# Optimization experiments

Measured on AMD Instinct MI355X. Metric: run time of the kernel, lower is better.

The kernel has to match this reference:

```python
import jax, jax.numpy as jnp
import numpy as np

N_GROUPS = 32  # getGroupSize(.) assumed -> channels // 8 (or //24 for 3*ch) == 32 for ch=256
HEADS = 4


def group_norm(x, gamma, beta, groups=N_GROUPS, eps=1e-5):
    n, c = x.shape
    xg = x.reshape(n, groups, c // groups)
    mu = xg.mean(-1, keepdims=True)
    var = xg.var(-1, keepdims=True)
    xn = ((xg - mu) * jax.lax.rsqrt(var + eps)).reshape(n, c)
    return xn * gamma + beta


def setup_inputs():
    key = jax.random.key(0)
    N, E, CH, HID = 2000, 16000, 256, 256
    ks = jax.random.split(key, 24)

    def w(k, shape, s=0.02):
        return (jax.random.normal(k, shape) * s).astype(jnp.float32)

    inp = {
        'x': jax.random.normal(ks[0], (N, CH), jnp.float32),
        'edge_index': jax.random.randint(ks[1], (2, E), 0, N),
        'edge_attr': jax.random.normal(ks[2], (E, CH), jnp.float32),
        # edge_mlp: GN(3ch)+ReLU -> Linear(3ch,hid) -> GN(hid)+ReLU -> Linear(hid,ch)
        'gn_e1_g': jnp.ones((3 * CH,), jnp.float32), 'gn_e1_b': jnp.zeros((3 * CH,), jnp.float32),
        'We1': w(ks[3], (3 * CH, HID)), 'be1': jnp.zeros((HID,), jnp.float32),
        'gn_e2_g': jnp.ones((HID,), jnp.float32), 'gn_e2_b': jnp.zeros((HID,), jnp.float32),
        'We2': w(ks[4], (HID, CH)), 'be2': jnp.zeros((CH,), jnp.float32),
        # actN: GN(ch)+ReLU
        'gn_n_g': jnp.ones((CH,), jnp.float32), 'gn_n_b': jnp.zeros((CH,), jnp.float32),
        # multi-head attention projections
        'Wq': w(ks[5], (CH, CH)), 'bq': jnp.zeros((CH,), jnp.float32),
        'Wk': w(ks[6], (CH, CH)), 'bk': jnp.zeros((CH,), jnp.float32),
        'Wv': w(ks[7], (CH, CH)), 'bv': jnp.zeros((CH,), jnp.float32),
        'Wo': w(ks[8], (CH, CH)), 'bo': jnp.zeros((CH,), jnp.float32),
        # node_mlp: Linear(2ch,hid) -> GN(hid)+ReLU -> Linear(hid,ch)
        'Wn1': w(ks[9], (2 * CH, HID)), 'bn1': jnp.zeros((HID,), jnp.float32),
        'gn_n2_g': jnp.ones((HID,), jnp.float32), 'gn_n2_b': jnp.zeros((HID,), jnp.float32),
        'Wn2': w(ks[10], (HID, CH)), 'bn2': jnp.zeros((CH,), jnp.float32),
    }
    return inp


def reference(x, edge_index, edge_attr,
              gn_e1_g, gn_e1_b, We1, be1, gn_e2_g, gn_e2_b, We2, be2,
              gn_n_g, gn_n_b, Wq, bq, Wk, bk, Wv, bv, Wo, bo,
              Wn1, bn1, gn_n2_g, gn_n2_b, Wn2, bn2):
    row, col = edge_index[0], edge_index[1]
    N, ch = x.shape
    E = edge_attr.shape[0]
    dk = ch // HEADS

    # ---- edge model: cat(src, tgt, e) -> GN/ReLU -> Lin -> GN/ReLU -> Lin (+res) ----
    e_in = jnp.concatenate([x[row], x[col], edge_attr], axis=1)  # [E, 3ch]
    h = jax.nn.relu(group_norm(e_in, gn_e1_g, gn_e1_b))
    h = h @ We1 + be1
    h = jax.nn.relu(group_norm(h, gn_e2_g, gn_e2_b))
    e_out = h @ We2 + be2 + edge_attr  # [E, ch]

    # ---- node model: dense-masked MHA, queries=nodes, keys/values=edges ----
    mask = jnp.zeros((N, E), x.dtype).at[col, jnp.arange(E)].set(1.0)  # scatter adjacency
    q = (x @ Wq + bq).reshape(N, HEADS, dk)
    k = (e_out @ Wk + bk).reshape(E, HEADS, dk)
    v = (e_out @ Wv + bv).reshape(E, HEADS, dk)
    scores = jnp.einsum('nhd,ehd->hne', q, k) / jnp.sqrt(jnp.float32(dk))  # [H, N, E]
    scores = jnp.where(mask[None] > 0, scores, jnp.float32(-1e9))
    attn = jax.nn.softmax(scores, axis=-1)
    g = jnp.einsum('hne,ehd->nhd', attn, v).reshape(N, ch) @ Wo + bo  # [N, ch]

    xa = jax.nn.relu(group_norm(x, gn_n_g, gn_n_b))
    h = jnp.concatenate([xa, g], axis=1) @ Wn1 + bn1  # thinker='cat'
    h = jax.nn.relu(group_norm(h, gn_n2_g, gn_n2_b))
    n_out = h @ Wn2 + bn2 + x  # residual

    return n_out, e_out
```

## Files before the change

### kernel.cpp

```cpp
#include <hip/hip_runtime.h>
#include <hip/hip_bf16.h>
#include <stdint.h>
#include <math.h>

#define CH 256

typedef __attribute__((ext_vector_type(8)))  short short8;
typedef __attribute__((ext_vector_type(16))) short short16;
typedef __attribute__((ext_vector_type(4)))  float f32x4;

#define GL2LDS16(g, l) __builtin_amdgcn_global_load_lds(                       \
    (const __attribute__((address_space(1))) void*)(g),                        \
    (__attribute__((address_space(3))) void*)(l), 16, 0, 0)

__device__ inline short f2bf(float f) {
    __hip_bfloat16 h = __float2bfloat16(f);
    short s;
    __builtin_memcpy(&s, &h, 2);
    return s;
}

__device__ inline float bf2f(short s) {
    unsigned u = ((unsigned)(unsigned short)s) << 16;
    float f;
    __builtin_memcpy(&f, &u, 4);
    return f;
}

__device__ inline float warp_sum64(float v) {
    v += __shfl_xor(v, 32, 64);
    v += __shfl_xor(v, 16, 64);
    v += __shfl_xor(v, 8, 64);
    v += __shfl_xor(v, 4, 64);
    v += __shfl_xor(v, 2, 64);
    v += __shfl_xor(v, 1, 64);
    return v;
}

__device__ inline float warp_max64(float v) {
    v = fmaxf(v, __shfl_xor(v, 32, 64));
    v = fmaxf(v, __shfl_xor(v, 16, 64));
    v = fmaxf(v, __shfl_xor(v, 8, 64));
    v = fmaxf(v, __shfl_xor(v, 4, 64));
    v = fmaxf(v, __shfl_xor(v, 2, 64));
    v = fmaxf(v, __shfl_xor(v, 1, 64));
    return v;
}

struct GArgs {
    const short* A; const short* Bt; const float* bias; const float* res;
    float* C; short* Cbf;
    const float* gamma; const float* beta; float* vbar;
    int M, K, Nc, ldc, coff;
    const short* A2; const short* Bt2; const float* bias2; short* Cbf2;
    int M2, Nc2, y_split;
    const float* x; const float* eattr; const int* rowi; const int* coli;
    const float* mu; const float* rs; const float* vg; const float* vbt;
};

template <int BM, int BN, int AMODE, int EPI, int DUAL, int VB>
__global__ __launch_bounds__(256) void mfma_gemm(GArgs g)
{
    constexpr int BK = 64;
    constexpr int AK = AMODE ? (BK + 8) : BK;
    constexpr int HM = BM / 2, HN = BN / 2;
    constexpr int FM = HM / 16, FN = HN / 16;
    constexpr int PA = BM / 32;
    constexpr int PB = BN / 32;
    __shared__ short As[BM * AK];
    __shared__ short Bs[BN * BK];
    __shared__ int sidx[AMODE ? 2 * BM : 1];

    const short* A = g.A; const short* Bt = g.Bt;
    const float* bias = g.bias; const float* res = g.res;
    float* C = g.C; short* Cbf = g.Cbf;
    int M = g.M, ldc = g.ldc, co = g.coff;
    const int K = g.K;
    int by = blockIdx.y, bx = blockIdx.x;
    bool qrole = false;
    if constexpr (DUAL) {
        if (by >= g.y_split) {
            by -= g.y_split;
            if (bx * BN >= g.Nc2) return;
            qrole = true;
            A = g.A2; Bt = g.Bt2; bias = g.bias2; Cbf = g.Cbf2;
            C = nullptr; res = nullptr;
            M = g.M2; ldc = g.Nc2; co = 0;
        }
    }

    const int t = threadIdx.x;
    const int wave = t >> 6, lane = t & 63;
    const int q = lane >> 4, l16 = lane & 15;
    const int row0 = by * BM;
    const int col0 = bx * BN;
    const int wm = wave & 1, wn = wave >> 1;

    if constexpr (AMODE) {
        if (t < BM) {
            int gr = row0 + t; if (gr >= M) gr = M - 1;
            sidx[t] = g.rowi[gr];
            sidx[BM + t] = g.coli[gr];
        }
        __syncthreads();
    }

    f32x4 acc[FM][FN];
    #pragma unroll
    for (int i = 0; i < FM; i++)
        #pragma unroll
        for (int j = 0; j < FN; j++) acc[i][j] = (f32x4){0.f, 0.f, 0.f, 0.f};

    for (int k0 = 0; k0 < K; k0 += BK) {
        if constexpr (AMODE == 1) {
            int reg = k0 >> 8;
            int rloc = t >> 3;
            int cpos = (t & 7) * 8;
            int pos = k0 + cpos;
            int G = pos / 24;
            float4 ga  = *(const float4*)&g.vg[pos];
            float4 ga2 = *(const float4*)&g.vg[pos + 4];
            float4 gb  = *(const float4*)&g.vbt[pos];
            float4 gb2 = *(const float4*)&g.vbt[pos + 4];
            int off = pos & 255;
            #pragma unroll
            for (int p = 0; p < BM / 32; p++) {
                int r2 = p * 32 + rloc;
                int e = row0 + r2; if (e >= M) e = M - 1;
                const float* srow;
                if (reg == 0)      srow = g.x + (size_t)sidx[r2] * CH;
                else if (reg == 1) srow = g.x + (size_t)sidx[BM + r2] * CH;
                else               srow = g.eattr + (size_t)e * CH;
                float4 va  = *(const float4*)&srow[off];
                float4 vb4 = *(const float4*)&srow[off + 4];
                float mm = g.mu[(size_t)e * 32 + G];
                float rr = g.rs[(size_t)e * 32 + G];
                short8 o;
                o[0] = f2bf(fmaxf((va.x - mm) * rr * ga.x + gb.x, 0.f));
                o[1] = f2bf(fmaxf((va.y - mm) * rr * ga.y + gb.y, 0.f));
                o[2] = f2bf(fmaxf((va.z - mm) * rr * ga.z + gb.z, 0.f));
                o[3] = f2bf(fmaxf((va.w - mm) * rr * ga.w + gb.w, 0.f));
                o[4] = f2bf(fmaxf((vb4.x - mm) * rr * ga2.x + gb2.x, 0.f));
                o[5] = f2bf(fmaxf((vb4.y - mm) * rr * ga2.y + gb2.y, 0.f));
                o[6] = f2bf(fmaxf((vb4.z - mm) * rr * ga2.z + gb2.z, 0.f));
                o[7] = f2bf(fmaxf((vb4.w - mm) * rr * ga2.w + gb2.w, 0.f));
                *(short8*)&As[r2 * AK + cpos] = o;
            }
        } else {
            #pragma unroll
            for (int p = 0; p < PA; p++) {
                int chunk = p * 256 + t;
                int r = chunk >> 3;
                int cs = (((chunk & 7) ^ (r & 7)) * 8);
                int gr = row0 + r; if (gr >= M) gr = M - 1;
                const short* gsrc = A + (size_t)gr * K + k0 + cs;
                short* ldst = &As[(p * 256 + wave * 64) * 8];
                GL2LDS16(gsrc, ldst);
            }
        }
        #pragma unroll
        for (int p = 0; p < PB; p++) {
            int chunk = p * 256 + t;
            int r = chunk >> 3;
            int cs = (((chunk & 7) ^ (r & 7)) * 8);
            const short* gsrc = Bt + (size_t)(col0 + r) * K + k0 + cs;
            short* ldst = &Bs[(p * 256 + wave * 64) * 8];
            GL2LDS16(gsrc, ldst);
        }
        __syncthreads();
        #pragma unroll
        for (int ks = 0; ks < 2; ks++) {
            short8 af[FM], bf[FN];
            #pragma unroll
            for (int mi = 0; mi < FM; mi++) {
                int R = wm * HM + mi * 16 + l16;
                if constexpr (AMODE == 1)
                    af[mi] = *(const short8*)&As[R * AK + ks * 32 + q * 8];
                else {
                    int slot = ((ks * 4 + q) ^ (R & 7)) * 8;
                    af[mi] = *(const short8*)&As[R * BK + slot];
                }
            }
            #pragma unroll
            for (int ni = 0; ni < FN; ni++) {
                int R = wn * HN + ni * 16 + l16;
                int slot = ((ks * 4 + q) ^ (R & 7)) * 8;
                bf[ni] = *(const short8*)&Bs[R * BK + slot];
            }
            #pragma unroll
            for (int mi = 0; mi < FM; mi++)
                #pragma unroll
                for (int ni = 0; ni < FN; ni++)
                    acc[mi][ni] = __builtin_amdgcn_mfma_f32_16x16x32_bf16(
                        af[mi], bf[ni], acc[mi][ni], 0, 0, 0);
        }
        __syncthreads();
    }

    #pragma unroll
    for (int ni = 0; ni < FN; ni++) {
        int cg = col0 + wn * HN + ni * 16 + l16;
        float bv = bias[cg];
        if constexpr (EPI == 1) {
            float ga = g.gamma[cg], be = g.beta[cg];
            #pragma unroll
            for (int mi = 0; mi < FM; mi++) {
                #pragma unroll
                for (int r = 0; r < 4; r++) {
                    float v = acc[mi][ni][r] + bv;
                    float s = v, sq = v * v;
                    s += __shfl_xor(s, 1, 64);  sq += __shfl_xor(sq, 1, 64);
                    s += __shfl_xor(s, 2, 64);  sq += __shfl_xor(sq, 2, 64);
                    s += __shfl_xor(s, 4, 64);  sq += __shfl_xor(sq, 4, 64);
                    float mean = s * 0.125f;
                    float var = sq * 0.125f - mean * mean;
                    float o = fmaxf((v - mean) * rsqrtf(var + 1e-5f) * ga + be, 0.f);
                    int rg = row0 + wm * HM + mi * 16 + q * 4 + r;
                    if (rg < M) Cbf[(size_t)rg * ldc + co + cg] = f2bf(o);
                }
            }
        } else {
            #pragma unroll
            for (int mi = 0; mi < FM; mi++) {
                #pragma unroll
                for (int r = 0; r < 4; r++) {
                    int rg = row0 + wm * HM + mi * 16 + q * 4 + r;
                    if (rg < M) {
                        float v = acc[mi][ni][r] + bv;
                        if (res) v += res[(size_t)rg * ldc + co + cg];
                        if (C)   C[(size_t)rg * ldc + co + cg] = v;
                        if (Cbf) Cbf[(size_t)rg * ldc + co + cg] = f2bf(v);
                    }
                }
            }
            if constexpr (VB) {
                if (!qrole && cg >= 256) {
                    float part = 0.f;
                    #pragma unroll
                    for (int mi = 0; mi < FM; mi++)
                        #pragma unroll
                        for (int r = 0; r < 4; r++) {
                            int rg = row0 + wm * HM + mi * 16 + q * 4 + r;
                            if (rg < M) part += acc[mi][ni][r] + bv;
                        }
                    part += __shfl_xor(part, 16, 64);
                    part += __shfl_xor(part, 32, 64);
                    if (q == 0) atomicAdd(&g.vbar[cg - 256], part);
                }
            }
        }
    }
}

struct PrepPack {
    const float* wsrc[8];
    short* wdst[8];
    int wK[8];
    int wstart[8];
    int NW, NP;
    const float* x;
    short* x_bf;
    short* cat_bf;
    float2* xs;
    const float* gng;
    const float* gnb;
    float* vbar;
    const float* bk;
    const float* bv;
    float* bkv;
    int* counts;
    int N;
};

__global__ __launch_bounds__(256) void prep_kernel(PrepPack p)
{
    int bid = blockIdx.x;
    int t = threadIdx.x;
    if (bid < p.NW) {
        int m = 0;
        #pragma unroll
        for (int i = 1; i < 8; i++) if (bid >= p.wstart[i]) m = i;
        int k0 = (bid - p.wstart[m]) * 16;
        const float* src = p.wsrc[m];
        short16 o;
        #pragma unroll
        for (int j = 0; j < 16; j++) o[j] = f2bf(src[(size_t)(k0 + j) * 256 + t]);
        *(short16*)(p.wdst[m] + (size_t)t * p.wK[m] + k0) = o;
        return;
    }
    if (bid >= p.NW + p.NP) {
        int i = (bid - p.NW - p.NP) * 256 + t;
        if (i < p.N) p.counts[i] = 0;
        return;
    }
    int pb = bid - p.NW;
    if (pb == 0) {
        p.vbar[t] = 0.f;
        p.bkv[t] = p.bk[t];
        p.bkv[256 + t] = p.bv[t];
    }
    int r = pb * 8 + (t >> 5);
    int g = t & 31;
    if (r >= p.N) return;
    size_t xb = (size_t)r * CH + g * 8;
    float4 a = *(const float4*)&p.x[xb];
    float4 b = *(const float4*)&p.x[xb + 4];
    short8 xr;
    xr[0] = f2bf(a.x); xr[1] = f2bf(a.y); xr[2] = f2bf(a.z); xr[3] = f2bf(a.w);
    xr[4] = f2bf(b.x); xr[5] = f2bf(b.y); xr[6] = f2bf(b.z); xr[7] = f2bf(b.w);
    *(short8*)&p.x_bf[xb] = xr;
    float s  = a.x + a.y + a.z + a.w + b.x + b.y + b.z + b.w;
    float s2 = a.x*a.x + a.y*a.y + a.z*a.z + a.w*a.w
             + b.x*b.x + b.y*b.y + b.z*b.z + b.w*b.w;
    p.xs[(size_t)r * 32 + g] = make_float2(s, s2);
    float m = s * 0.125f;
    float var = s2 * 0.125f - m * m;
    float rsd = rsqrtf(var + 1e-5f);
    float4 g0 = *(const float4*)&p.gng[g * 8];
    float4 g1 = *(const float4*)&p.gng[g * 8 + 4];
    float4 b0 = *(const float4*)&p.gnb[g * 8];
    float4 b1 = *(const float4*)&p.gnb[g * 8 + 4];
    short8 o;
    o[0] = f2bf(fmaxf((a.x - m) * rsd * g0.x + b0.x, 0.f));
    o[1] = f2bf(fmaxf((a.y - m) * rsd * g0.y + b0.y, 0.f));
    o[2] = f2bf(fmaxf((a.z - m) * rsd * g0.z + b0.z, 0.f));
    o[3] = f2bf(fmaxf((a.w - m) * rsd * g0.w + b0.w, 0.f));
    o[4] = f2bf(fmaxf((b.x - m) * rsd * g1.x + b1.x, 0.f));
    o[5] = f2bf(fmaxf((b.y - m) * rsd * g1.y + b1.y, 0.f));
    o[6] = f2bf(fmaxf((b.z - m) * rsd * g1.z + b1.z, 0.f));
    o[7] = f2bf(fmaxf((b.w - m) * rsd * g1.w + b1.w, 0.f));
    *(short8*)&p.cat_bf[(size_t)r * (2 * CH) + g * 8] = o;
}

__global__ __launch_bounds__(256) void estats_kernel(
    const float* __restrict__ eattr, const int* __restrict__ rowi,
    const int* __restrict__ coli, const float2* __restrict__ xs,
    float* __restrict__ mu, float* __restrict__ rs,
    int* __restrict__ counts, int E)
{
    __shared__ float2 ea[8][32];
    int t = threadIdx.x;
    int slot = t >> 5, g = t & 31;
    int e = blockIdx.x * 8 + slot;
    float4 a = *(const float4*)&eattr[(size_t)e * CH + g * 8];
    float4 b = *(const float4*)&eattr[(size_t)e * CH + g * 8 + 4];
    float s  = a.x + a.y + a.z + a.w + b.x + b.y + b.z + b.w;
    float s2 = a.x*a.x + a.y*a.y + a.z*a.z + a.w*a.w
             + b.x*b.x + b.y*b.y + b.z*b.z + b.w*b.w;
    ea[slot][g] = make_float2(s, s2);
    int r = rowi[e], c = coli[e];
    if (g == 0) atomicAdd(&counts[c], 1);
    __syncthreads();
    float S = 0.f, S2 = 0.f;
    #pragma unroll
    for (int j = 0; j < 3; j++) {
        int b3 = 3 * g + j;
        int src = b3 >> 5, idx = b3 & 31;
        float2 v;
        if (src == 0)      v = xs[(size_t)r * 32 + idx];
        else if (src == 1) v = xs[(size_t)c * 32 + idx];
        else               v = ea[slot][idx];
        S += v.x; S2 += v.y;
    }
    float m = S * (1.f / 24.f);
    float var = S2 * (1.f / 24.f) - m * m;
    mu[(size_t)e * 32 + g] = m;
    rs[(size_t)e * 32 + g] = rsqrtf(var + 1e-5f);
}

__global__ __launch_bounds__(1024) void scan_kernel(
    const int* __restrict__ counts, int* __restrict__ offsets,
    int* __restrict__ cursor, int N)
{
    __shared__ int s[1024];
    int t = threadIdx.x;
    int a = (2 * t     < N) ? counts[2 * t]     : 0;
    int b = (2 * t + 1 < N) ? counts[2 * t + 1] : 0;
    s[t] = a + b;
    __syncthreads();
    for (int off = 1; off < 1024; off <<= 1) {
        int v = (t >= off) ? s[t - off] : 0;
        __syncthreads();
        s[t] += v;
        __syncthreads();
    }
    int excl = (t > 0) ? s[t - 1] : 0;
    if (2 * t < N)     { offsets[2 * t]     = excl;     cursor[2 * t]     = excl; }
    if (2 * t + 1 < N) { offsets[2 * t + 1] = excl + a; cursor[2 * t + 1] = excl + a; }
    if (t == 1023) offsets[N] = s[1023];
}

__global__ __launch_bounds__(256) void escore_kernel(
    const short* __restrict__ qb, const short* __restrict__ kvb,
    const int* __restrict__ coli, int* __restrict__ cursor,
    int* __restrict__ elist, float* __restrict__ sc, int E)
{
    int e = blockIdx.x * 4 + (threadIdx.x >> 6);
    int lane = threadIdx.x & 63;
    if (e >= E) return;
    int c = coli[e];
    if (lane == 0) { int p = atomicAdd(&cursor[c], 1); elist[p] = e; }
    const short* qrow = qb + (size_t)c * CH;
    const short* krow = kvb + (size_t)e * 512;
    float d0 = bf2f(qrow[lane])       * bf2f(krow[lane]);
    float d1 = bf2f(qrow[64 + lane])  * bf2f(krow[64 + lane]);
    float d2 = bf2f(qrow[128 + lane]) * bf2f(krow[128 + lane]);
    float d3 = bf2f(qrow[192 + lane]) * bf2f(krow[192 + lane]);
    d0 = warp_sum64(d0);
    d1 = warp_sum64(d1);
    d2 = warp_sum64(d2);
    d3 = warp_sum64(d3);
    if (lane == 0) {
        float4 o = {d0 * 0.125f, d1 * 0.125f, d2 * 0.125f, d3 * 0.125f};
        *(float4*)&sc[(size_t)e * 4] = o;
    }
}

__global__ __launch_bounds__(256) void attn_kernel(
    const float* __restrict__ sc, const short* __restrict__ kvb,
    const int* __restrict__ offsets, const int* __restrict__ elist,
    const float* __restrict__ vbar, short* __restrict__ g_bf, int N, int E)
{
    int n = blockIdx.x;
    int h = threadIdx.x >> 6;
    int lane = threadIdx.x & 63;
    int s0 = offsets[n], s1 = offsets[n + 1];
    float out = 0.f;
    if (s1 > s0) {
        float m = -INFINITY, l = 0.f;
        for (int base = s0; base < s1; base += 64) {
            int cn = s1 - base; if (cn > 64) cn = 64;
            int e = (lane < cn) ? elist[base + lane] : 0;
            float s = (lane < cn) ? sc[(size_t)e * 4 + h] : -INFINITY;
            float mc = warp_max64(s);
            float nm = fmaxf(m, mc);
            float scale = __expf(m - nm);
            float pp = (lane < cn) ? __expf(s - nm) : 0.f;
            float ps = warp_sum64(pp);
            l = l * scale + ps;
            out *= scale;
            m = nm;
            for (int i = 0; i < cn; i++) {
                float pi = __shfl(pp, i, 64);
                int   ei = __shfl(e, i, 64);
                out += pi * bf2f(kvb[(size_t)ei * 512 + 256 + h * 64 + lane]);
            }
        }
        out /= l;
    } else {
        out = vbar[h * 64 + lane] * (1.f / (float)E);
    }
    g_bf[(size_t)n * CH + h * 64 + lane] = f2bf(out);
}

extern "C" void kernel_launch(void* const* d_in, const int* in_sizes, int n_in,
                              void* d_out, int out_size, void* d_ws, size_t ws_size,
                              hipStream_t stream)
{
    const float* x       = (const float*)d_in[0];
    const int*   ei      = (const int*)d_in[1];
    const float* eattr   = (const float*)d_in[2];
    const float* gn_e1_g = (const float*)d_in[3];
    const float* gn_e1_b = (const float*)d_in[4];
    const float* We1     = (const float*)d_in[5];
    const float* be1     = (const float*)d_in[6];
    const float* gn_e2_g = (const float*)d_in[7];
    const float* gn_e2_b = (const float*)d_in[8];
    const float* We2     = (const float*)d_in[9];
    const float* be2     = (const float*)d_in[10];
    const float* gn_n_g  = (const float*)d_in[11];
    const float* gn_n_b  = (const float*)d_in[12];
    const float* Wq      = (const float*)d_in[13];
    const float* bq      = (const float*)d_in[14];
    const float* Wk      = (const float*)d_in[15];
    const float* bk      = (const float*)d_in[16];
    const float* Wv      = (const float*)d_in[17];
    const float* bv      = (const float*)d_in[18];
    const float* Wo      = (const float*)d_in[19];
    const float* bo      = (const float*)d_in[20];
    const float* Wn1     = (const float*)d_in[21];
    const float* bn1     = (const float*)d_in[22];
    const float* gn_n2_g = (const float*)d_in[23];
    const float* gn_n2_b = (const float*)d_in[24];
    const float* Wn2     = (const float*)d_in[25];
    const float* bn2     = (const float*)d_in[26];

    const int N = in_sizes[0] / CH;
    const int E = in_sizes[2] / CH;

    float* nout = (float*)d_out;
    float* eout = (float*)d_out + (size_t)N * CH;

    char* base = (char*)d_ws;
    short* kv_bf  = (short*)base; base += (size_t)E * 512 * 2;
    short* h2_bf  = (short*)base; base += (size_t)E * CH * 2;
    short* eo_bf  = (short*)base; base += (size_t)E * CH * 2;
    short* q_bf   = (short*)base; base += (size_t)N * CH * 2;
    short* g_bf   = (short*)base; base += (size_t)N * CH * 2;
    short* cat_bf = (short*)base; base += (size_t)N * 2 * CH * 2;
    short* hn_bf  = (short*)base; base += (size_t)N * CH * 2;
    short* x_bf   = (short*)base; base += (size_t)N * CH * 2;
    float2* xs    = (float2*)base; base += (size_t)N * 32 * 8;
    float* mub    = (float*)base; base += (size_t)E * 32 * 4;
    float* rsb    = (float*)base; base += (size_t)E * 32 * 4;
    float* sc     = (float*)base; base += (size_t)E * 4 * 4;
    float* vbar   = (float*)base; base += 1024;
    float* bkv    = (float*)base; base += 2048;
    short* We1t = (short*)base; base += (size_t)768 * 256 * 2;
    short* We2t = (short*)base; base += (size_t)256 * 256 * 2;
    short* Wqt  = (short*)base; base += (size_t)256 * 256 * 2;
    short* Wkvt = (short*)base; base += (size_t)512 * 256 * 2;
    short* Wot  = (short*)base; base += (size_t)256 * 256 * 2;
    short* Wn1t = (short*)base; base += (size_t)512 * 256 * 2;
    short* Wn2t = (short*)base; base += (size_t)256 * 256 * 2;
    int* counts  = (int*)base;
    int* offsets = counts + N;
    int* cursor  = offsets + (N + 1) + 3;
    int* elist   = cursor + N;

    const int* rowi = ei;
    const int* coli = ei + E;

    dim3 blk(256);

    PrepPack pp;
    const float* wsrc[8] = {We1, We2, Wq, Wk, Wv, Wo, Wn1, Wn2};
    short* wdst[8] = {We1t, We2t, Wqt, Wkvt, Wkvt + (size_t)256 * 256, Wot, Wn1t, Wn2t};
    const int wKd[8] = {768, 256, 256, 256, 256, 256, 512, 256};
    int acc = 0;
    for (int i = 0; i < 8; i++) {
        pp.wsrc[i] = wsrc[i]; pp.wdst[i] = wdst[i]; pp.wK[i] = wKd[i];
        pp.wstart[i] = acc; acc += wKd[i] / 16;
    }
    pp.NW = acc;
    pp.NP = (N + 7) / 8;
    pp.x = x; pp.x_bf = x_bf; pp.cat_bf = cat_bf; pp.xs = xs;
    pp.gng = gn_n_g; pp.gnb = gn_n_b;
    pp.vbar = vbar; pp.bk = bk; pp.bv = bv; pp.bkv = bkv;
    pp.counts = counts; pp.N = N;
    int nzero = (N + 255) / 256;
    prep_kernel<<<pp.NW + pp.NP + nzero, blk, 0, stream>>>(pp);

    estats_kernel<<<E / 8, blk, 0, stream>>>(eattr, rowi, coli, xs, mub, rsb, counts, E);
    scan_kernel<<<1, 1024, 0, stream>>>(counts, offsets, cursor, N);

    GArgs ga = {};
    ga.Bt = We1t; ga.bias = be1; ga.Cbf = h2_bf;
    ga.gamma = gn_e2_g; ga.beta = gn_e2_b;
    ga.M = E; ga.K = 3 * CH; ga.Nc = CH; ga.ldc = CH; ga.coff = 0;
    ga.x = x; ga.eattr = eattr; ga.rowi = rowi; ga.coli = coli;
    ga.mu = mub; ga.rs = rsb; ga.vg = gn_e1_g; ga.vbt = gn_e1_b;
    mfma_gemm<128, 64, 1, 1, 0, 0><<<dim3(4, E / 128), blk, 0, stream>>>(ga);

    ga = {};
    ga.A = h2_bf; ga.Bt = We2t; ga.bias = be2; ga.res = eattr;
    ga.C = eout; ga.Cbf = eo_bf;
    ga.M = E; ga.K = CH; ga.Nc = CH; ga.ldc = CH; ga.coff = 0;
    mfma_gemm<64, 64, 0, 0, 0, 0><<<dim3(4, E / 64), blk, 0, stream>>>(ga);

    ga = {};
    ga.A = eo_bf; ga.Bt = Wkvt; ga.bias = bkv; ga.Cbf = kv_bf; ga.vbar = vbar;
    ga.M = E; ga.K = CH; ga.Nc = 512; ga.ldc = 512; ga.coff = 0;
    ga.A2 = x_bf; ga.Bt2 = Wqt; ga.bias2 = bq; ga.Cbf2 = q_bf;
    ga.M2 = N; ga.Nc2 = CH; ga.y_split = E / 64;
    mfma_gemm<64, 64, 0, 0, 1, 1><<<dim3(8, E / 64 + (N + 63) / 64), blk, 0, stream>>>(ga);

    escore_kernel<<<(E + 3) / 4, blk, 0, stream>>>(q_bf, kv_bf, coli, cursor, elist, sc, E);
    attn_kernel<<<N, blk, 0, stream>>>(sc, kv_bf, offsets, elist, vbar, g_bf, N, E);

    ga = {};
    ga.A = g_bf; ga.Bt = Wot; ga.bias = bo; ga.Cbf = cat_bf;
    ga.M = N; ga.K = CH; ga.Nc = CH; ga.ldc = 2 * CH; ga.coff = CH;
    mfma_gemm<64, 64, 0, 0, 0, 0><<<dim3(4, (N + 63) / 64), blk, 0, stream>>>(ga);

    ga = {};
    ga.A = cat_bf; ga.Bt = Wn1t; ga.bias = bn1; ga.Cbf = hn_bf;
    ga.gamma = gn_n2_g; ga.beta = gn_n2_b;
    ga.M = N; ga.K = 2 * CH; ga.Nc = CH; ga.ldc = CH; ga.coff = 0;
    mfma_gemm<64, 64, 0, 1, 0, 0><<<dim3(4, (N + 63) / 64), blk, 0, stream>>>(ga);

    ga = {};
    ga.A = hn_bf; ga.Bt = Wn2t; ga.bias = bn2; ga.res = x; ga.C = nout;
    ga.M = N; ga.K = CH; ga.Nc = CH; ga.ldc = CH; ga.coff = 0;
    mfma_gemm<64, 64, 0, 0, 0, 0><<<dim3(4, (N + 63) / 64), blk, 0, stream>>>(ga);
}
```

Baseline: 262.1 us.

## Gather bf16 copies of x and edge_attr in edge GEMM; shrink GEMM row tiles

```diff
diff --git a/kernel.cpp b/kernel.cpp
--- a/kernel.cpp
+++ b/kernel.cpp
@@ -54,7 +54,7 @@
     int M, K, Nc, ldc, coff;
     const short* A2; const short* Bt2; const float* bias2; short* Cbf2;
     int M2, Nc2, y_split;
-    const float* x; const float* eattr; const int* rowi; const int* coli;
+    const short* xbf; const short* eabf; const int* rowi; const int* coli;
     const float* mu; const float* rs; const float* vg; const float* vbt;
 };
 
@@ -115,8 +115,8 @@
         if constexpr (AMODE == 1) {
             int reg = k0 >> 8;
             int rloc = t >> 3;
-            int cpos = (t & 7) * 8;
-            int pos = k0 + cpos;
+            int c8 = (t & 7) * 8;
+            int pos = k0 + c8;
             int G = pos / 24;
             float4 ga  = *(const float4*)&g.vg[pos];
             float4 ga2 = *(const float4*)&g.vg[pos + 4];
@@ -127,24 +127,23 @@
             for (int p = 0; p < BM / 32; p++) {
                 int r2 = p * 32 + rloc;
                 int e = row0 + r2; if (e >= M) e = M - 1;
-                const float* srow;
-                if (reg == 0)      srow = g.x + (size_t)sidx[r2] * CH;
-                else if (reg == 1) srow = g.x + (size_t)sidx[BM + r2] * CH;
-                else               srow = g.eattr + (size_t)e * CH;
-                float4 va  = *(const float4*)&srow[off];
-                float4 vb4 = *(const float4*)&srow[off + 4];
+                const short* srow;
+                if (reg == 0)      srow = g.xbf + (size_t)sidx[r2] * CH;
+                else if (reg == 1) srow = g.xbf + (size_t)sidx[BM + r2] * CH;
+                else               srow = g.eabf + (size_t)e * CH;
+                short8 v8 = *(const short8*)&srow[off];
                 float mm = g.mu[(size_t)e * 32 + G];
                 float rr = g.rs[(size_t)e * 32 + G];
                 short8 o;
-                o[0] = f2bf(fmaxf((va.x - mm) * rr * ga.x + gb.x, 0.f));
-                o[1] = f2bf(fmaxf((va.y - mm) * rr * ga.y + gb.y, 0.f));
-                o[2] = f2bf(fmaxf((va.z - mm) * rr * ga.z + gb.z, 0.f));
-                o[3] = f2bf(fmaxf((va.w - mm) * rr * ga.w + gb.w, 0.f));
-                o[4] = f2bf(fmaxf((vb4.x - mm) * rr * ga2.x + gb2.x, 0.f));
-                o[5] = f2bf(fmaxf((vb4.y - mm) * rr * ga2.y + gb2.y, 0.f));
-                o[6] = f2bf(fmaxf((vb4.z - mm) * rr * ga2.z + gb2.z, 0.f));
-                o[7] = f2bf(fmaxf((vb4.w - mm) * rr * ga2.w + gb2.w, 0.f));
-                *(short8*)&As[r2 * AK + cpos] = o;
+                o[0] = f2bf(fmaxf((bf2f(v8[0]) - mm) * rr * ga.x + gb.x, 0.f));
+                o[1] = f2bf(fmaxf((bf2f(v8[1]) - mm) * rr * ga.y + gb.y, 0.f));
+                o[2] = f2bf(fmaxf((bf2f(v8[2]) - mm) * rr * ga.z + gb.z, 0.f));
+                o[3] = f2bf(fmaxf((bf2f(v8[3]) - mm) * rr * ga.w + gb.w, 0.f));
+                o[4] = f2bf(fmaxf((bf2f(v8[4]) - mm) * rr * ga2.x + gb2.x, 0.f));
+                o[5] = f2bf(fmaxf((bf2f(v8[5]) - mm) * rr * ga2.y + gb2.y, 0.f));
+                o[6] = f2bf(fmaxf((bf2f(v8[6]) - mm) * rr * ga2.z + gb2.z, 0.f));
+                o[7] = f2bf(fmaxf((bf2f(v8[7]) - mm) * rr * ga2.w + gb2.w, 0.f));
+                *(short8*)&As[r2 * AK + c8] = o;
             }
         } else {
             #pragma unroll
@@ -336,7 +335,7 @@
     const float* __restrict__ eattr, const int* __restrict__ rowi,
     const int* __restrict__ coli, const float2* __restrict__ xs,
     float* __restrict__ mu, float* __restrict__ rs,
-    int* __restrict__ counts, int E)
+    short* __restrict__ eabf, int* __restrict__ counts, int E)
 {
     __shared__ float2 ea[8][32];
     int t = threadIdx.x;
@@ -344,6 +343,10 @@
     int e = blockIdx.x * 8 + slot;
     float4 a = *(const float4*)&eattr[(size_t)e * CH + g * 8];
     float4 b = *(const float4*)&eattr[(size_t)e * CH + g * 8 + 4];
+    short8 o8;
+    o8[0] = f2bf(a.x); o8[1] = f2bf(a.y); o8[2] = f2bf(a.z); o8[3] = f2bf(a.w);
+    o8[4] = f2bf(b.x); o8[5] = f2bf(b.y); o8[6] = f2bf(b.z); o8[7] = f2bf(b.w);
+    *(short8*)&eabf[(size_t)e * CH + g * 8] = o8;
     float s  = a.x + a.y + a.z + a.w + b.x + b.y + b.z + b.w;
     float s2 = a.x*a.x + a.y*a.y + a.z*a.z + a.w*a.w
              + b.x*b.x + b.y*b.y + b.z*b.z + b.w*b.w;
@@ -495,6 +498,7 @@
     short* kv_bf  = (short*)base; base += (size_t)E * 512 * 2;
     short* h2_bf  = (short*)base; base += (size_t)E * CH * 2;
     short* eo_bf  = (short*)base; base += (size_t)E * CH * 2;
+    short* eabf   = (short*)base; base += (size_t)E * CH * 2;
     short* q_bf   = (short*)base; base += (size_t)N * CH * 2;
     short* g_bf   = (short*)base; base += (size_t)N * CH * 2;
     short* cat_bf = (short*)base; base += (size_t)N * 2 * CH * 2;
@@ -541,16 +545,17 @@
     int nzero = (N + 255) / 256;
     prep_kernel<<<pp.NW + pp.NP + nzero, blk, 0, stream>>>(pp);
 
-    estats_kernel<<<E / 8, blk, 0, stream>>>(eattr, rowi, coli, xs, mub, rsb, counts, E);
+    estats_kernel<<<E / 8, blk, 0, stream>>>(eattr, rowi, coli, xs, mub, rsb,
+                                             eabf, counts, E);
     scan_kernel<<<1, 1024, 0, stream>>>(counts, offsets, cursor, N);
 
     GArgs ga = {};
     ga.Bt = We1t; ga.bias = be1; ga.Cbf = h2_bf;
     ga.gamma = gn_e2_g; ga.beta = gn_e2_b;
     ga.M = E; ga.K = 3 * CH; ga.Nc = CH; ga.ldc = CH; ga.coff = 0;
-    ga.x = x; ga.eattr = eattr; ga.rowi = rowi; ga.coli = coli;
+    ga.xbf = x_bf; ga.eabf = eabf; ga.rowi = rowi; ga.coli = coli;
     ga.mu = mub; ga.rs = rsb; ga.vg = gn_e1_g; ga.vbt = gn_e1_b;
-    mfma_gemm<128, 64, 1, 1, 0, 0><<<dim3(4, E / 128), blk, 0, stream>>>(ga);
+    mfma_gemm<64, 64, 1, 1, 0, 0><<<dim3(4, E / 64), blk, 0, stream>>>(ga);
 
     ga = {};
     ga.A = h2_bf; ga.Bt = We2t; ga.bias = be2; ga.res = eattr;
@@ -571,16 +576,16 @@
     ga = {};
     ga.A = g_bf; ga.Bt = Wot; ga.bias = bo; ga.Cbf = cat_bf;
     ga.M = N; ga.K = CH; ga.Nc = CH; ga.ldc = 2 * CH; ga.coff = CH;
-    mfma_gemm<64, 64, 0, 0, 0, 0><<<dim3(4, (N + 63) / 64), blk, 0, stream>>>(ga);
+    mfma_gemm<32, 64, 0, 0, 0, 0><<<dim3(4, (N + 31) / 32), blk, 0, stream>>>(ga);
 
     ga = {};
     ga.A = cat_bf; ga.Bt = Wn1t; ga.bias = bn1; ga.Cbf = hn_bf;
     ga.gamma = gn_n2_g; ga.beta = gn_n2_b;
     ga.M = N; ga.K = 2 * CH; ga.Nc = CH; ga.ldc = CH; ga.coff = 0;
-    mfma_gemm<64, 64, 0, 1, 0, 0><<<dim3(4, (N + 63) / 64), blk, 0, stream>>>(ga);
+    mfma_gemm<32, 64, 0, 1, 0, 0><<<dim3(4, (N + 31) / 32), blk, 0, stream>>>(ga);
 
     ga = {};
     ga.A = hn_bf; ga.Bt = Wn2t; ga.bias = bn2; ga.res = x; ga.C = nout;
     ga.M = N; ga.K = CH; ga.Nc = CH; ga.ldc = CH; ga.coff = 0;
-    mfma_gemm<64, 64, 0, 0, 0, 0><<<dim3(4, (N + 63) / 64), blk, 0, stream>>>(ga);
-}
+    mfma_gemm<32, 64, 0, 0, 0, 0><<<dim3(4, (N + 31) / 32), blk, 0, stream>>>(ga);
+}
```

Result: faster. 239.1 us (-8.8%).
